# Kernel tuning notes

Hardware: AMD Instinct MI355X
Metric: run time of the kernel (lower is better)

## Reference

```python
import jax, jax.numpy as jnp
import numpy as np

VOCAB = 1_000_000
EMBED = 128
N_DENSE = 13
N_SPARSE = 26
BATCH = 16384
BOT_DIMS = [512, 256, 128]
TOP_DIMS = [1024, 1024, 512, 256, 1]


def setup_inputs() -> dict:
    key = jax.random.key(0)
    ks = list(jax.random.split(key, 32))
    # input: 13 dense floats + 26 categorical ids (stored as floats, cast in fwd)
    dense = jax.random.normal(ks[0], (BATCH, N_DENSE), dtype=jnp.float32)
    cat = jax.random.randint(ks[1], (BATCH, N_SPARSE), 0, VOCAB).astype(jnp.float32)
    x = jnp.concatenate([dense, cat], axis=1)
    inp = {"x": x, "train": 0}
    # bottom MLP params
    fan_in = N_DENSE
    for i, d in enumerate(BOT_DIMS):
        s = (6.0 / (fan_in + d)) ** 0.5  # glorot uniform scale
        inp[f"bw{i}"] = jax.random.uniform(ks[2 + 2 * i], (fan_in, d), jnp.float32, -s, s)
        inp[f"bb{i}"] = jax.random.normal(ks[3 + 2 * i], (d,), jnp.float32) * (1.0 / d) ** 0.5
        fan_in = d
    # unified embedding table
    inp["emb"] = jax.random.uniform(ks[10], (VOCAB, EMBED), jnp.float32) / jnp.sqrt(float(VOCAB))
    # top MLP params; input dim = embed_dim + triu(27) = 128 + 378 = 506
    n_feat = 1 + N_SPARSE  # bottom output contributes one 128-dim feature row
    fan_in = EMBED + (n_feat * (n_feat + 1)) // 2
    for i, d in enumerate(TOP_DIMS):
        std = (2.0 / (fan_in + d)) ** 0.5
        inp[f"tw{i}"] = jax.random.normal(ks[12 + 2 * i], (fan_in, d), jnp.float32) * std
        inp[f"tb{i}"] = jax.random.normal(ks[13 + 2 * i], (d,), jnp.float32) * (1.0 / d) ** 0.5
        fan_in = d
    return inp


def dot_interact(f):
    # f: [B, n, d]; keep_diags=True -> upper-triangular (incl. diag) of f @ f^T
    n = f.shape[1]
    iu, ju = jnp.triu_indices(n)
    xact = jnp.einsum('bnd,bmd->bnm', f, f)  # [B, n, n]
    return xact[:, iu, ju]  # [B, n*(n+1)/2]


def reference(x, train, bw0, bb0, bw1, bb1, bw2, bb2, emb,
              tw0, tb0, tw1, tb1, tw2, tb2, tw3, tb3, tw4, tb4):
    del train
    dense, cat = jnp.split(x, [N_DENSE], axis=1)
    idx = jnp.reshape(cat.astype(jnp.int32), [-1]) % VOCAB
    # bottom MLP
    h = dense
    for w, b in ((bw0, bb0), (bw1, bb1), (bw2, bb2)):
        h = jax.nn.relu(h @ w + b)
    bot_out = h  # [B, 128]
    B = bot_out.shape[0]
    feat = jnp.reshape(bot_out, [B, -1, EMBED])  # [B, 1, 128]
    embf = jnp.reshape(emb[idx], [B, -1, EMBED])  # [B, 26, 128]
    feat = jnp.concatenate([feat, embf], axis=1)  # [B, 27, 128]
    inter = dot_interact(feat)  # [B, 378]
    t = jnp.concatenate([bot_out, inter], axis=-1)  # [B, 506]
    tops = [(tw0, tb0), (tw1, tb1), (tw2, tb2), (tw3, tb3), (tw4, tb4)]
    for i, (w, b) in enumerate(tops):
        t = t @ w + b
        if i < len(tops) - 1:
            t = jax.nn.relu(t)
    return t  # [B, 1] logits
```

## Files before the change

kernel.cpp:

```cpp
#include <hip/hip_runtime.h>

typedef float v4f  __attribute__((ext_vector_type(4)));
typedef __bf16 bf16x8 __attribute__((ext_vector_type(8)));

__device__ __forceinline__ unsigned short f2bf(float f) {
    unsigned u = __builtin_bit_cast(unsigned, f);
    u += 0x7FFFu + ((u >> 16) & 1u);
    return (unsigned short)(u >> 16);
}
__device__ __forceinline__ float bf2f(unsigned short h) {
    return __builtin_bit_cast(float, (unsigned)h << 16);
}

__device__ __forceinline__ void gload16(const unsigned short* g, unsigned short* l) {
    __builtin_amdgcn_global_load_lds(
        (const __attribute__((address_space(1))) unsigned int*)g,
        (__attribute__((address_space(3))) unsigned int*)l, 16, 0, 0);
}

#define M_BATCH 16384

__global__ __launch_bounds__(256) void wprep(const float* __restrict__ in,
                                             unsigned short* __restrict__ out,
                                             int K, int N, int Kpad) {
    __shared__ float tile[32][33];
    int tx = threadIdx.x & 31;
    int ty = threadIdx.x >> 5;
    int n0 = blockIdx.x * 32, k0 = blockIdx.y * 32;
#pragma unroll
    for (int i = 0; i < 32; i += 8) {
        int k = k0 + ty + i, n = n0 + tx;
        tile[ty + i][tx] = (k < K && n < N) ? in[(size_t)k * N + n] : 0.f;
    }
    __syncthreads();
#pragma unroll
    for (int i = 0; i < 32; i += 8) {
        int n = n0 + ty + i, k = k0 + tx;
        if (n < N && k < Kpad) out[(size_t)n * Kpad + k] = f2bf(tile[tx][ty + i]);
    }
}

__global__ __launch_bounds__(256) void bot0(const float* __restrict__ x,
                                            const float* __restrict__ w,
                                            const float* __restrict__ b,
                                            unsigned short* __restrict__ h0) {
    int gid = blockIdx.x * 256 + threadIdx.x;
    int row = gid >> 9, col = gid & 511;
    const float* xr = x + (size_t)row * 39;
    float acc = b[col];
#pragma unroll
    for (int k = 0; k < 13; k++) acc += xr[k] * w[k * 512 + col];
    h0[gid] = f2bf(fmaxf(acc, 0.f));
}

__global__ __launch_bounds__(256) void gemm_bt(const unsigned short* __restrict__ A,
                                               const unsigned short* __restrict__ Bt,
                                               const float* __restrict__ bias,
                                               unsigned short* __restrict__ C,
                                               int N, int K, int relu) {
    __shared__ __align__(16) unsigned short As[128 * 32];
    __shared__ __align__(16) unsigned short Bs[128 * 32];
    const int tid  = threadIdx.x;
    const int wave = tid >> 6, lane = tid & 63;
    const int quad = lane >> 4, r16 = lane & 15;
    const int m_blk = blockIdx.y * 128, n_blk = blockIdx.x * 128;
    const int w_m = (wave >> 1) * 64, w_n = (wave & 1) * 64;

    v4f acc[4][4] = {};

    const int slot0 = tid, slot1 = tid + 256;
    const int rowS0 = slot0 >> 2, chS0 = slot0 & 3;
    const int rowS1 = slot1 >> 2, chS1 = slot1 & 3;

    const unsigned short* pa0 = A  + (size_t)(m_blk + rowS0) * K + chS0 * 8;
    const unsigned short* pa1 = A  + (size_t)(m_blk + rowS1) * K + chS1 * 8;
    const unsigned short* pb0 = Bt + (size_t)(n_blk + rowS0) * K + chS0 * 8;
    const unsigned short* pb1 = Bt + (size_t)(n_blk + rowS1) * K + chS1 * 8;

    unsigned short* lA0 = As + slot0 * 8;
    unsigned short* lA1 = As + slot1 * 8;
    unsigned short* lB0 = Bs + slot0 * 8;
    unsigned short* lB1 = Bs + slot1 * 8;

    for (int k0 = 0; k0 < K; k0 += 32) {
        gload16(pa0 + k0, lA0);
        gload16(pa1 + k0, lA1);
        gload16(pb0 + k0, lB0);
        gload16(pb1 + k0, lB1);
        __syncthreads();
        bf16x8 af[4], bf[4];
#pragma unroll
        for (int i = 0; i < 4; i++)
            af[i] = *(const bf16x8*)(As + (w_m + i * 16 + r16) * 32 + quad * 8);
#pragma unroll
        for (int j = 0; j < 4; j++)
            bf[j] = *(const bf16x8*)(Bs + (w_n + j * 16 + r16) * 32 + quad * 8);
#pragma unroll
        for (int i = 0; i < 4; i++)
#pragma unroll
            for (int j = 0; j < 4; j++)
                acc[i][j] = __builtin_amdgcn_mfma_f32_16x16x32_bf16(af[i], bf[j], acc[i][j], 0, 0, 0);
        __syncthreads();
    }

#pragma unroll
    for (int j = 0; j < 4; j++) {
        int gcol = n_blk + w_n + j * 16 + r16;
        float bv = bias[gcol];
#pragma unroll
        for (int i = 0; i < 4; i++) {
            int grow = m_blk + w_m + i * 16 + quad * 4;
#pragma unroll
            for (int r = 0; r < 4; r++) {
                float v = acc[i][j][r] + bv;
                if (relu) v = fmaxf(v, 0.f);
                C[(size_t)(grow + r) * N + gcol] = f2bf(v);
            }
        }
    }
}

#define FS 136
__global__ __launch_bounds__(256) void interact(const float* __restrict__ x,
                                                const float* __restrict__ emb,
                                                const unsigned short* __restrict__ h2,
                                                unsigned short* __restrict__ top_in) {
    __shared__ __align__(16) unsigned short feat[4][32 * FS];
    __shared__ __align__(16) unsigned short rowb[4][512];
    const int wave = threadIdx.x >> 6, lane = threadIdx.x & 63;
    const int s = blockIdx.x * 4 + wave;
    unsigned short* fw = feat[wave];
    unsigned short* rb = rowb[wave];
    const int quad = lane >> 4, r16 = lane & 15;

    int cat = 0;
    if (lane < 26) cat = (int)x[(size_t)s * 39 + 13 + lane];
    if (lane < 16)
        *(uint4*)(fw + lane * 8) = *(const uint4*)(h2 + (size_t)s * 128 + lane * 8);
#pragma unroll
    for (int i = 0; i < 13; i++) {
        int t = i * 64 + lane;
        int row = t >> 5, c4 = t & 31;
        int id = __shfl(cat, row);
        float4 v = *(const float4*)(emb + (size_t)id * 128 + c4 * 4);
        ushort4 o;
        o.x = f2bf(v.x); o.y = f2bf(v.y); o.z = f2bf(v.z); o.w = f2bf(v.w);
        *(ushort4*)(fw + (size_t)(row + 1) * FS + c4 * 4) = o;
    }
    v4f c00 = {0,0,0,0}, c01 = {0,0,0,0}, c11 = {0,0,0,0};
#pragma unroll
    for (int kc = 0; kc < 4; kc++) {
        bf16x8 a0 = *(const bf16x8*)(fw + r16 * FS + kc * 32 + quad * 8);
        bf16x8 a1 = *(const bf16x8*)(fw + (16 + r16) * FS + kc * 32 + quad * 8);
        c00 = __builtin_amdgcn_mfma_f32_16x16x32_bf16(a0, a0, c00, 0, 0, 0);
        c01 = __builtin_amdgcn_mfma_f32_16x16x32_bf16(a0, a1, c01, 0, 0, 0);
        c11 = __builtin_amdgcn_mfma_f32_16x16x32_bf16(a1, a1, c11, 0, 0, 0);
    }
    if (lane < 16) *(uint4*)(rb + lane * 8) = *(const uint4*)(fw + lane * 8);
    if (lane < 6) rb[506 + lane] = 0;
#pragma unroll
    for (int r = 0; r < 4; r++) {
        int i = quad * 4 + r;
        int j = r16;
        if (i <= j)
            rb[128 + i * 27 - (i * (i - 1)) / 2 + (j - i)] = f2bf(c00[r]);
        int j2 = 16 + r16;
        if (j2 < 27) {
            rb[128 + i * 27 - (i * (i - 1)) / 2 + (j2 - i)] = f2bf(c01[r]);
            int ii = 16 + quad * 4 + r;
            if (ii <= j2)
                rb[128 + ii * 27 - (ii * (ii - 1)) / 2 + (j2 - ii)] = f2bf(c11[r]);
        }
    }
    *(uint4*)(top_in + (size_t)s * 512 + lane * 8) = *(const uint4*)(rb + lane * 8);
}

__global__ __launch_bounds__(256) void top_final(const unsigned short* __restrict__ ht3,
                                                 const float* __restrict__ w,
                                                 const float* __restrict__ b,
                                                 float* __restrict__ out) {
    int wave = threadIdx.x >> 6, lane = threadIdx.x & 63;
    int row = blockIdx.x * 4 + wave;
    ushort4 av = *(const ushort4*)(ht3 + (size_t)row * 256 + lane * 4);
    float4 wv = *(const float4*)(w + lane * 4);
    float s = bf2f(av.x) * wv.x + bf2f(av.y) * wv.y + bf2f(av.z) * wv.z + bf2f(av.w) * wv.w;
#pragma unroll
    for (int off = 32; off; off >>= 1) s += __shfl_down(s, off);
    if (lane == 0) out[row] = s + b[0];
}

extern "C" void kernel_launch(void* const* d_in, const int* in_sizes, int n_in,
                              void* d_out, int out_size, void* d_ws, size_t ws_size,
                              hipStream_t stream) {
    (void)in_sizes; (void)n_in; (void)out_size; (void)ws_size;
    const float* x   = (const float*)d_in[0];
    const float* bw0 = (const float*)d_in[2];
    const float* bb0 = (const float*)d_in[3];
    const float* bw1 = (const float*)d_in[4];
    const float* bb1 = (const float*)d_in[5];
    const float* bw2 = (const float*)d_in[6];
    const float* bb2 = (const float*)d_in[7];
    const float* emb = (const float*)d_in[8];
    const float* tw0 = (const float*)d_in[9];
    const float* tb0 = (const float*)d_in[10];
    const float* tw1 = (const float*)d_in[11];
    const float* tb1 = (const float*)d_in[12];
    const float* tw2 = (const float*)d_in[13];
    const float* tb2 = (const float*)d_in[14];
    const float* tw3 = (const float*)d_in[15];
    const float* tb3 = (const float*)d_in[16];
    const float* tw4 = (const float*)d_in[17];
    const float* tb4 = (const float*)d_in[18];
    float* out = (float*)d_out;

    char* ws = (char*)d_ws;
    size_t off = 0;
    auto alloc = [&](size_t bytes) {
        void* p = ws + off;
        off += (bytes + 255) & ~(size_t)255;
        return p;
    };
    unsigned short* bw1t = (unsigned short*)alloc((size_t)256 * 512 * 2);
    unsigned short* bw2t = (unsigned short*)alloc((size_t)128 * 256 * 2);
    unsigned short* tw0t = (unsigned short*)alloc((size_t)1024 * 512 * 2);
    unsigned short* tw1t = (unsigned short*)alloc((size_t)1024 * 1024 * 2);
    unsigned short* tw2t = (unsigned short*)alloc((size_t)512 * 1024 * 2);
    unsigned short* tw3t = (unsigned short*)alloc((size_t)256 * 512 * 2);
    unsigned short* h2   = (unsigned short*)alloc((size_t)M_BATCH * 128 * 2);
    unsigned short* bufA = (unsigned short*)alloc((size_t)M_BATCH * 1024 * 2);
    unsigned short* bufB = (unsigned short*)alloc((size_t)M_BATCH * 1024 * 2);

    unsigned short* h0     = bufA;
    unsigned short* h1     = bufB;
    unsigned short* top_in = bufA;
    unsigned short* ht0    = bufB;
    unsigned short* ht1    = bufA;
    unsigned short* ht2    = bufB;
    unsigned short* ht3    = bufA;

    dim3 blk(256);
    wprep<<<dim3(256 / 32,  512 / 32),  blk, 0, stream>>>(bw1,  bw1t, 512,  256,  512);
    wprep<<<dim3(128 / 32,  256 / 32),  blk, 0, stream>>>(bw2,  bw2t, 256,  128,  256);
    wprep<<<dim3(1024 / 32, 512 / 32),  blk, 0, stream>>>(tw0,  tw0t, 506,  1024, 512);
    wprep<<<dim3(1024 / 32, 1024 / 32), blk, 0, stream>>>(tw1,  tw1t, 1024, 1024, 1024);
    wprep<<<dim3(512 / 32,  1024 / 32), blk, 0, stream>>>(tw2,  tw2t, 1024, 512,  1024);
    wprep<<<dim3(256 / 32,  512 / 32),  blk, 0, stream>>>(tw3,  tw3t, 512,  256,  512);

    bot0<<<dim3(M_BATCH * 512 / 256), blk, 0, stream>>>(x, bw0, bb0, h0);
    gemm_bt<<<dim3(256 / 128, M_BATCH / 128), blk, 0, stream>>>(h0, bw1t, bb1, h1, 256, 512, 1);
    gemm_bt<<<dim3(128 / 128, M_BATCH / 128), blk, 0, stream>>>(h1, bw2t, bb2, h2, 128, 256, 1);

    interact<<<dim3(M_BATCH / 4), blk, 0, stream>>>(x, emb, h2, top_in);

    gemm_bt<<<dim3(1024 / 128, M_BATCH / 128), blk, 0, stream>>>(top_in, tw0t, tb0, ht0, 1024, 512, 1);
    gemm_bt<<<dim3(1024 / 128, M_BATCH / 128), blk, 0, stream>>>(ht0, tw1t, tb1, ht1, 1024, 1024, 1);
    gemm_bt<<<dim3(512 / 128,  M_BATCH / 128), blk, 0, stream>>>(ht1, tw2t, tb2, ht2, 512, 1024, 1);
    gemm_bt<<<dim3(256 / 128,  M_BATCH / 128), blk, 0, stream>>>(ht2, tw3t, tb3, ht3, 256, 512, 1);
    top_final<<<dim3(M_BATCH / 4), blk, 0, stream>>>(ht3, tw4, tb4, out);
}
```

Baseline: 849.3 us.

## Double-buffer LDS tiles in bf16 MFMA GEMM to overlap loads with compute

The GEMM main loop now uses two LDS buffers for the A and B tiles. It issues the direct global-to-LDS loads for the next K slice before running MFMAs on the current slice, with one vmcnt drain plus barrier per slice. The aim is to hide global load latency that previously stalled each iteration, where a load was always followed by a barrier before compute. It doubles LDS use per block, which may reduce occupancy, and the loop now assumes K is a multiple of 64.

```diff
diff --git a/kernel.cpp b/kernel.cpp
--- a/kernel.cpp
+++ b/kernel.cpp
@@ -58,8 +58,10 @@
                                                const float* __restrict__ bias,
                                                unsigned short* __restrict__ C,
                                                int N, int K, int relu) {
-    __shared__ __align__(16) unsigned short As[128 * 32];
-    __shared__ __align__(16) unsigned short Bs[128 * 32];
+    __shared__ __align__(16) unsigned short As0[128 * 32];
+    __shared__ __align__(16) unsigned short Bs0[128 * 32];
+    __shared__ __align__(16) unsigned short As1[128 * 32];
+    __shared__ __align__(16) unsigned short Bs1[128 * 32];
     const int tid  = threadIdx.x;
     const int wave = tid >> 6, lane = tid & 63;
     const int quad = lane >> 4, r16 = lane & 15;
@@ -77,31 +79,52 @@
     const unsigned short* pb0 = Bt + (size_t)(n_blk + rowS0) * K + chS0 * 8;
     const unsigned short* pb1 = Bt + (size_t)(n_blk + rowS1) * K + chS1 * 8;
 
-    unsigned short* lA0 = As + slot0 * 8;
-    unsigned short* lA1 = As + slot1 * 8;
-    unsigned short* lB0 = Bs + slot0 * 8;
-    unsigned short* lB1 = Bs + slot1 * 8;
-
-    for (int k0 = 0; k0 < K; k0 += 32) {
-        gload16(pa0 + k0, lA0);
-        gload16(pa1 + k0, lA1);
-        gload16(pb0 + k0, lB0);
-        gload16(pb1 + k0, lB1);
-        __syncthreads();
-        bf16x8 af[4], bf[4];
-#pragma unroll
-        for (int i = 0; i < 4; i++)
-            af[i] = *(const bf16x8*)(As + (w_m + i * 16 + r16) * 32 + quad * 8);
-#pragma unroll
-        for (int j = 0; j < 4; j++)
-            bf[j] = *(const bf16x8*)(Bs + (w_n + j * 16 + r16) * 32 + quad * 8);
-#pragma unroll
-        for (int i = 0; i < 4; i++)
-#pragma unroll
-            for (int j = 0; j < 4; j++)
-                acc[i][j] = __builtin_amdgcn_mfma_f32_16x16x32_bf16(af[i], bf[j], acc[i][j], 0, 0, 0);
-        __syncthreads();
-    }
+#define STAGE(AsX, BsX, kk)                                   \
+    do {                                                      \
+        gload16(pa0 + (kk), AsX + slot0 * 8);                 \
+        gload16(pa1 + (kk), AsX + slot1 * 8);                 \
+        gload16(pb0 + (kk), BsX + slot0 * 8);                 \
+        gload16(pb1 + (kk), BsX + slot1 * 8);                 \
+    } while (0)
+
+#define DRAIN_BAR()                                           \
+    do {                                                      \
+        asm volatile("s_waitcnt vmcnt(0)" ::: "memory");      \
+        __builtin_amdgcn_s_barrier();                         \
+        __builtin_amdgcn_sched_barrier(0);                    \
+    } while (0)
+
+#define COMPUTE(AsX, BsX)                                                         \
+    do {                                                                          \
+        bf16x8 af[4], bf[4];                                                      \
+        _Pragma("unroll")                                                         \
+        for (int i = 0; i < 4; i++)                                               \
+            af[i] = *(const bf16x8*)(AsX + (w_m + i * 16 + r16) * 32 + quad * 8); \
+        _Pragma("unroll")                                                         \
+        for (int j = 0; j < 4; j++)                                               \
+            bf[j] = *(const bf16x8*)(BsX + (w_n + j * 16 + r16) * 32 + quad * 8); \
+        _Pragma("unroll")                                                         \
+        for (int i = 0; i < 4; i++)                                               \
+            _Pragma("unroll")                                                     \
+            for (int j = 0; j < 4; j++)                                           \
+                acc[i][j] = __builtin_amdgcn_mfma_f32_16x16x32_bf16(              \
+                    af[i], bf[j], acc[i][j], 0, 0, 0);                            \
+    } while (0)
+
+    STAGE(As0, Bs0, 0);
+    DRAIN_BAR();
+
+    for (int k0 = 0; k0 < K; k0 += 64) {
+        STAGE(As1, Bs1, k0 + 32);
+        COMPUTE(As0, Bs0);
+        DRAIN_BAR();
+        if (k0 + 64 < K) STAGE(As0, Bs0, k0 + 64);
+        COMPUTE(As1, Bs1);
+        DRAIN_BAR();
+    }
+#undef STAGE
+#undef DRAIN_BAR
+#undef COMPUTE
 
 #pragma unroll
     for (int j = 0; j < 4; j++) {
```

Result: no change. 847.3 us (-0.2%).
